# Optimization experiments

Measured on AMD Instinct MI355X. Metric: run time of the kernel, lower is better.

## Reference

```python
import jax, jax.numpy as jnp
import numpy as np

B, K, C = 16384, 128, 32  # batch, feature dim, number of private-label classes
LN2 = 0.6931471805599453


def setup_inputs() -> dict:
    key = jax.random.key(0)
    k1, k2, k3 = jax.random.split(key, 3)
    feature = jax.random.normal(k1, (B, K), dtype=jnp.float32)
    privatelabel = jax.random.randint(k2, (B,), 0, C)
    pan = jax.random.normal(k3, (1,), dtype=jnp.float32)  # unused by the module
    return {"feature": feature, "privatelabel": privatelabel, "pan": pan}


def _privacy_loss(feature, privatelabel):
    b, k = feature.shape
    labels = privatelabel
    onehot = jax.nn.one_hot(labels, C, dtype=feature.dtype)          # [B,C]
    counts = onehot.sum(axis=0)                                      # [C]
    mu = (onehot.T @ feature) / counts[:, None]                      # [C,K] per-class mean
    xc = feature - mu[labels]                                        # [B,K] centered rows
    # per-class scatter: S_c = (1/n_c) * sum_{i in c} xc_i xc_i^T + I
    xw = xc[:, None, :] * onehot[:, :, None]                         # [B,C,K]
    S = jnp.einsum('bci,bj->cij', xw, xc) / counts[:, None, None]
    S = S + jnp.eye(k, dtype=feature.dtype)                          # Sigma_a = I
    # pairwise Gaussian KL (with log base 2, as in the torch code)
    ld2 = jnp.linalg.slogdet(S)[1] / LN2                             # log2 det Sigma_c
    inv = jnp.linalg.inv(S)                                          # [C,K,K]
    diff = mu[:, None, :] - mu[None, :, :]                           # [C,C,K] (i,j)
    quad = jnp.einsum('ijk,jkl,ijl->ij', diff, inv, diff)           # (u1-u2)^T S2^-1 (u1-u2)
    tr = jnp.einsum('jab,iba->ij', inv, S)                           # trace(S2^-1 S1)
    kl = 0.5 * ((ld2[None, :] - ld2[:, None]) - float(k) + quad + tr)
    # dict-insertion key order = order of first occurrence of each label;
    # loops are i in [0, C-2] (rows), j in [1, C-1] (cols) over that order
    first = jnp.full((C,), b, dtype=jnp.int32).at[labels].min(
        jnp.arange(b, dtype=jnp.int32))
    rank = jnp.argsort(jnp.argsort(first))                           # appearance rank per class
    mask = (rank[:, None] <= C - 2) & (rank[None, :] >= 1)
    result = -jnp.sum(mu * mu) + jnp.sum(jnp.where(mask, kl, jnp.zeros_like(kl)))
    return result[None]                                              # shape (1,), like torch


def reference(feature, privatelabel, pan):
    return _privacy_loss(feature, privatelabel)
```

## Files before the change

### kernel.cpp

```cpp
#include <hip/hip_runtime.h>

#define B_ROWS 16384
#define K_DIM  128
#define C_CLS  32

#define O_COUNTS   0
#define O_FIRST    256
#define O_RANK     512
#define O_OFFS     768
#define O_KLACC    1024
#define O_LD2      1152
#define O_COUNTSF  1280
#define O_COLSUM   2048
#define O_MU       18432
#define O_LIST     34816
#define O_S        102400
#define O_PART     (102400 + 2097152)
#define O_INV      O_PART

__global__ __launch_bounds__(1024) void k_bucket(const int* __restrict__ label,
    int* __restrict__ counts, int* __restrict__ rank_g, int* __restrict__ offs,
    float* __restrict__ countsf, int* __restrict__ list) {
  __shared__ int lc[C_CLS], lf[C_CLS], loff[C_CLS], lcur[C_CLS];
  const int t = threadIdx.x;
  if (t < C_CLS) { lc[t] = 0; lf[t] = 0x7fffffff; lcur[t] = 0; }
  __syncthreads();
  #pragma unroll
  for (int q = 0; q < 16; ++q) {
    int i = q * 1024 + t;
    int c = label[i];
    atomicAdd(&lc[c], 1);
    atomicMin(&lf[c], i);
  }
  __syncthreads();
  if (t == 0) {
    int run = 0;
    for (int c = 0; c < C_CLS; ++c) { loff[c] = run; run += lc[c]; }
  }
  __syncthreads();
  if (t < C_CLS) {
    counts[t]  = lc[t];
    countsf[t] = (float)lc[t];
    offs[t]    = loff[t];
    int f = lf[t], r = 0;
    for (int c2 = 0; c2 < C_CLS; ++c2) {
      int f2 = lf[c2];
      r += (f2 < f) || (f2 == f && c2 < t);
    }
    rank_g[t] = r;
  }
  #pragma unroll
  for (int q = 0; q < 16; ++q) {
    int i = q * 1024 + t;
    int c = label[i];
    int pos = atomicAdd(&lcur[c], 1);
    list[loff[c] + pos] = i;
  }
}

__global__ __launch_bounds__(256) void k_scatter(const float* __restrict__ feat,
    const int* __restrict__ counts, const int* __restrict__ offs,
    const int* __restrict__ list, float* __restrict__ part, float* __restrict__ colsum) {
  const int c = blockIdx.x >> 2, s = blockIdx.x & 3;
  const int n = counts[c], off = offs[c];
  const int beg = off + (n * s) / 4, end = off + (n * (s + 1)) / 4;
  __shared__ __align__(16) float ls[32 * 128];
  const int t = threadIdx.x;
  const int tr = t >> 4, tc = t & 15;
  float acc[8][8];
  #pragma unroll
  for (int i = 0; i < 8; ++i)
    #pragma unroll
    for (int j = 0; j < 8; ++j) acc[i][j] = 0.f;
  float cs = 0.f;
  const int col = t & 127, half = t >> 7;
  for (int base = beg; base < end; base += 32) {
    const int nb = min(32, end - base);
    __syncthreads();
    #pragma unroll
    for (int w = 0; w < 4; ++w) {
      int f4 = w * 256 + t;
      int r = f4 >> 5, c4 = f4 & 31;
      float4 v = make_float4(0.f, 0.f, 0.f, 0.f);
      if (r < nb) {
        int row = list[base + r];
        v = ((const float4*)(feat + (long)row * K_DIM))[c4];
      }
      ((float4*)ls)[f4] = v;
    }
    __syncthreads();
    #pragma unroll
    for (int r0 = 0; r0 < 16; ++r0) cs += ls[(half * 16 + r0) * 128 + col];
    for (int r = 0; r < nb; ++r) {
      const float4* lr = (const float4*)(ls + r * 128);
      float4 A0 = lr[tr * 2], A1 = lr[tr * 2 + 1];
      float4 B0 = lr[tc * 2], B1 = lr[tc * 2 + 1];
      float av[8] = {A0.x, A0.y, A0.z, A0.w, A1.x, A1.y, A1.z, A1.w};
      float bv[8] = {B0.x, B0.y, B0.z, B0.w, B1.x, B1.y, B1.z, B1.w};
      #pragma unroll
      for (int i = 0; i < 8; ++i)
        #pragma unroll
        for (int j = 0; j < 8; ++j) acc[i][j] += av[i] * bv[j];
    }
  }
  float* Pc = part + (long)blockIdx.x * 16384;
  #pragma unroll
  for (int i = 0; i < 8; ++i) {
    float4* prow = (float4*)(Pc + (tr * 8 + i) * 128);
    prow[tc * 2]     = make_float4(acc[i][0], acc[i][1], acc[i][2], acc[i][3]);
    prow[tc * 2 + 1] = make_float4(acc[i][4], acc[i][5], acc[i][6], acc[i][7]);
  }
  atomicAdd(&colsum[c * 128 + col], cs);
}

__global__ __launch_bounds__(256) void k_finalize(const float* __restrict__ part,
    float* __restrict__ S, const float* __restrict__ colsum,
    const float* __restrict__ countsf, float* __restrict__ mu) {
  const int c = blockIdx.x, t = threadIdx.x;
  __shared__ __align__(16) float ml[128];
  const float n = countsf[c];
  if (t < 128) {
    float m = colsum[c * 128 + t] / n;
    ml[t] = m;
    mu[c * 128 + t] = m;
  }
  __syncthreads();
  const float4* P0 = (const float4*)(part + (long)(c * 4 + 0) * 16384);
  const float4* P1 = (const float4*)(part + (long)(c * 4 + 1) * 16384);
  const float4* P2 = (const float4*)(part + (long)(c * 4 + 2) * 16384);
  const float4* P3 = (const float4*)(part + (long)(c * 4 + 3) * 16384);
  float4* S4 = (float4*)(S + c * 16384);
  const float rn = 1.0f / n;
  #pragma unroll
  for (int q = 0; q < 16; ++q) {
    int f4 = q * 256 + t;
    int a = f4 >> 5, b = (f4 & 31) * 4;
    float4 v0 = P0[f4], v1 = P1[f4], v2 = P2[f4], v3 = P3[f4];
    float4 v;
    v.x = (v0.x + v1.x) + (v2.x + v3.x);
    v.y = (v0.y + v1.y) + (v2.y + v3.y);
    v.z = (v0.z + v1.z) + (v2.z + v3.z);
    v.w = (v0.w + v1.w) + (v2.w + v3.w);
    float ma = ml[a];
    v.x = v.x * rn - ma * ml[b + 0] + ((a == b + 0) ? 1.f : 0.f);
    v.y = v.y * rn - ma * ml[b + 1] + ((a == b + 1) ? 1.f : 0.f);
    v.z = v.z * rn - ma * ml[b + 2] + ((a == b + 2) ? 1.f : 0.f);
    v.w = v.w * rn - ma * ml[b + 3] + ((a == b + 3) ? 1.f : 0.f);
    S4[f4] = v;
  }
}

__global__ __launch_bounds__(512) void k_sweep(const float* __restrict__ S,
    float* __restrict__ INVg, float* __restrict__ ld2) {
  const int c = blockIdx.x, t = threadIdx.x;
  __shared__ __align__(16) float vbuf[2][132];
  const float4* S4 = (const float4*)(S + c * 16384);
  float4 A[8];
  #pragma unroll
  for (int q = 0; q < 8; ++q) A[q] = S4[q * 512 + t];
  const int h = t >> 5, c4i = t & 31;
  float lda = 0.f;

  for (int P = 0; P < 128; ++P) {
    float* vb = vbuf[P & 1];
    if (h == (P & 15)) {
      const int qexp = P >> 4;
      float4 ex = A[0];
      #pragma unroll
      for (int q = 1; q < 8; ++q) if (q == qexp) ex = A[q];
      if (c4i == (P >> 2)) {
        const int e = P & 3;
        float dv = (e == 0) ? ex.x : (e == 1) ? ex.y : (e == 2) ? ex.z : ex.w;
        vb[128] = dv;
        if (e == 0) ex.x -= 1.f; else if (e == 1) ex.y -= 1.f;
        else if (e == 2) ex.z -= 1.f; else ex.w -= 1.f;
      }
      ((float4*)vb)[c4i] = ex;
    }
    __syncthreads();
    const float d = vb[128];
    const float dinv = 1.0f / d;
    lda += __log2f(d);
    const float4 vc = ((const float4*)vb)[c4i];
    const float4 wc = make_float4(vc.x * dinv, vc.y * dinv, vc.z * dinv, vc.w * dinv);
    #pragma unroll
    for (int q = 0; q < 8; ++q) {
      const float vr = vb[q * 16 + h];
      A[q].x -= vr * wc.x;
      A[q].y -= vr * wc.y;
      A[q].z -= vr * wc.z;
      A[q].w -= vr * wc.w;
    }
  }

  float4* O4 = (float4*)(INVg + c * 16384);
  const int e = h & 3;
  const float4 addv = make_float4(e == 0 ? 2.f : 0.f, e == 1 ? 2.f : 0.f,
                                  e == 2 ? 2.f : 0.f, e == 3 ? 2.f : 0.f);
  #pragma unroll
  for (int q = 0; q < 8; ++q) {
    const int rq = q * 16 + h;
    const float pf = (c4i == (rq >> 2)) ? 1.f : 0.f;
    float4 o;
    o.x = pf * addv.x - A[q].x;
    o.y = pf * addv.y - A[q].y;
    o.z = pf * addv.z - A[q].z;
    o.w = pf * addv.w - A[q].w;
    O4[q * 512 + t] = o;
  }
  if (t == 0) ld2[c] = lda;
}

__global__ __launch_bounds__(256) void k_pairs(const float* __restrict__ S,
    const float* __restrict__ INVg, const float* __restrict__ mu,
    const float* __restrict__ ld2, const int* __restrict__ rank_g,
    float* __restrict__ klacc) {
  const int j = blockIdx.x, i = blockIdx.y;
  if (rank_g[i] > C_CLS - 2 || rank_g[j] < 1) return;
  __shared__ __align__(16) float dl[128];
  __shared__ float wsum[4];
  const int t = threadIdx.x;
  if (t < 128) dl[t] = mu[i * 128 + t] - mu[j * 128 + t];
  __syncthreads();
  const float4* Si4 = (const float4*)(S + i * 16384);
  const float4* Ij4 = (const float4*)(INVg + j * 16384);
  float s = 0.f;
  #pragma unroll
  for (int q = 0; q < 16; ++q) {
    int f4 = q * 256 + t;
    int a = f4 >> 5, b4 = f4 & 31;
    float da = dl[a];
    float4 db = ((const float4*)dl)[b4];
    float4 si = Si4[f4], ij = Ij4[f4];
    s += ij.x * (si.x + da * db.x);
    s += ij.y * (si.y + da * db.y);
    s += ij.z * (si.z + da * db.z);
    s += ij.w * (si.w + da * db.w);
  }
  #pragma unroll
  for (int off = 32; off > 0; off >>= 1) s += __shfl_xor(s, off);
  if ((t & 63) == 0) wsum[t >> 6] = s;
  __syncthreads();
  if (t == 0) {
    float tot = wsum[0] + wsum[1] + wsum[2] + wsum[3];
    float kl = 0.5f * ((ld2[j] - ld2[i]) - 128.0f + tot);
    atomicAdd(klacc, kl);
  }
}

__global__ __launch_bounds__(256) void k_final(const float* __restrict__ mu,
    const float* __restrict__ klacc, float* __restrict__ out) {
  const int t = threadIdx.x;
  __shared__ float wsum[4];
  float s = 0.f;
  #pragma unroll
  for (int q = 0; q < 16; ++q) {
    float m = mu[q * 256 + t];
    s += m * m;
  }
  #pragma unroll
  for (int off = 32; off > 0; off >>= 1) s += __shfl_xor(s, off);
  if ((t & 63) == 0) wsum[t >> 6] = s;
  __syncthreads();
  if (t == 0) out[0] = klacc[0] - (wsum[0] + wsum[1] + wsum[2] + wsum[3]);
}

extern "C" void kernel_launch(void* const* d_in, const int* in_sizes, int n_in,
                              void* d_out, int out_size, void* d_ws, size_t ws_size,
                              hipStream_t stream) {
  const float* feat  = (const float*)d_in[0];
  const int*   label = (const int*)d_in[1];
  float* out = (float*)d_out;
  char*  ws  = (char*)d_ws;

  int*   counts  = (int*)(ws + O_COUNTS);
  int*   rank_g  = (int*)(ws + O_RANK);
  int*   offs    = (int*)(ws + O_OFFS);
  float* klacc   = (float*)(ws + O_KLACC);
  float* ld2     = (float*)(ws + O_LD2);
  float* countsf = (float*)(ws + O_COUNTSF);
  float* colsum  = (float*)(ws + O_COLSUM);
  float* mu      = (float*)(ws + O_MU);
  int*   list    = (int*)(ws + O_LIST);
  float* S       = (float*)(ws + O_S);
  float* part    = (float*)(ws + O_PART);
  float* INVg    = (float*)(ws + O_INV);

  hipMemsetAsync(ws, 0, 18432, stream);

  k_bucket  <<<1,            1024, 0, stream>>>(label, counts, rank_g, offs, countsf, list);
  k_scatter <<<128,           256, 0, stream>>>(feat, counts, offs, list, part, colsum);
  k_finalize<<<C_CLS,         256, 0, stream>>>(part, S, colsum, countsf, mu);
  k_sweep   <<<C_CLS,         512, 0, stream>>>(S, INVg, ld2);
  k_pairs   <<<dim3(C_CLS, C_CLS), 256, 0, stream>>>(S, INVg, mu, ld2, rank_g, klacc);
  k_final   <<<1,             256, 0, stream>>>(mu, klacc, out);
}
```

Before: 180.0 us.

## Fuse label bucketing into scatter blocks and block the Gauss-Jordan sweep by four

New measurement: 201.9 us. 12.1% more time.

```diff
diff --git a/kernel.cpp b/kernel.cpp
--- a/kernel.cpp
+++ b/kernel.cpp
@@ -7,65 +7,52 @@
 #define O_COUNTS   0
 #define O_FIRST    256
 #define O_RANK     512
-#define O_OFFS     768
 #define O_KLACC    1024
 #define O_LD2      1152
-#define O_COUNTSF  1280
 #define O_COLSUM   2048
 #define O_MU       18432
-#define O_LIST     34816
 #define O_S        102400
 #define O_PART     (102400 + 2097152)
 #define O_INV      O_PART
 
-__global__ __launch_bounds__(1024) void k_bucket(const int* __restrict__ label,
-    int* __restrict__ counts, int* __restrict__ rank_g, int* __restrict__ offs,
-    float* __restrict__ countsf, int* __restrict__ list) {
-  __shared__ int lc[C_CLS], lf[C_CLS], loff[C_CLS], lcur[C_CLS];
+__global__ __launch_bounds__(256) void k_init(int* __restrict__ counts,
+    int* __restrict__ first, float* __restrict__ colsum, float* __restrict__ klacc) {
   const int t = threadIdx.x;
-  if (t < C_CLS) { lc[t] = 0; lf[t] = 0x7fffffff; lcur[t] = 0; }
-  __syncthreads();
-  #pragma unroll
-  for (int q = 0; q < 16; ++q) {
-    int i = q * 1024 + t;
-    int c = label[i];
-    atomicAdd(&lc[c], 1);
-    atomicMin(&lf[c], i);
-  }
-  __syncthreads();
-  if (t == 0) {
-    int run = 0;
-    for (int c = 0; c < C_CLS; ++c) { loff[c] = run; run += lc[c]; }
-  }
-  __syncthreads();
-  if (t < C_CLS) {
-    counts[t]  = lc[t];
-    countsf[t] = (float)lc[t];
-    offs[t]    = loff[t];
-    int f = lf[t], r = 0;
-    for (int c2 = 0; c2 < C_CLS; ++c2) {
-      int f2 = lf[c2];
-      r += (f2 < f) || (f2 == f && c2 < t);
-    }
-    rank_g[t] = r;
-  }
-  #pragma unroll
-  for (int q = 0; q < 16; ++q) {
-    int i = q * 1024 + t;
-    int c = label[i];
-    int pos = atomicAdd(&lcur[c], 1);
-    list[loff[c] + pos] = i;
-  }
+  if (t < C_CLS) { counts[t] = 0; first[t] = 0x7fffffff; }
+  if (t == 0) klacc[0] = 0.f;
+  for (int i = t; i < C_CLS * K_DIM; i += 256) colsum[i] = 0.f;
 }
 
 __global__ __launch_bounds__(256) void k_scatter(const float* __restrict__ feat,
-    const int* __restrict__ counts, const int* __restrict__ offs,
-    const int* __restrict__ list, float* __restrict__ part, float* __restrict__ colsum) {
+    const int* __restrict__ label, int* __restrict__ counts, int* __restrict__ first,
+    float* __restrict__ part, float* __restrict__ colsum) {
   const int c = blockIdx.x >> 2, s = blockIdx.x & 3;
-  const int n = counts[c], off = offs[c];
-  const int beg = off + (n * s) / 4, end = off + (n * (s + 1)) / 4;
+  __shared__ int lls[4096];
+  __shared__ int lcnt;
   __shared__ __align__(16) float ls[32 * 128];
   const int t = threadIdx.x;
+  if (t == 0) lcnt = 0;
+  __syncthreads();
+  int myMin = 0x7fffffff;
+  const int lane = t & 63;
+  for (int r0 = 0; r0 < 4096; r0 += 256) {
+    const int i = s * 4096 + r0 + t;
+    const bool match = (label[i] == c);
+    unsigned long long mask = __ballot(match);
+    int prefix = __popcll(mask & ((1ull << lane) - 1ull));
+    int wcnt = __popcll(mask);
+    int base = 0;
+    if (lane == 0 && wcnt) base = atomicAdd(&lcnt, wcnt);
+    base = __shfl(base, 0);
+    if (match) { lls[base + prefix] = i; myMin = min(myMin, i); }
+  }
+  #pragma unroll
+  for (int off = 32; off > 0; off >>= 1) myMin = min(myMin, __shfl_xor(myMin, off));
+  if (lane == 0 && myMin != 0x7fffffff) atomicMin(&first[c], myMin);
+  __syncthreads();
+  const int n = lcnt;
+  if (t == 0) atomicAdd(&counts[c], n);
+
   const int tr = t >> 4, tc = t & 15;
   float acc[8][8];
   #pragma unroll
@@ -74,8 +61,8 @@
     for (int j = 0; j < 8; ++j) acc[i][j] = 0.f;
   float cs = 0.f;
   const int col = t & 127, half = t >> 7;
-  for (int base = beg; base < end; base += 32) {
-    const int nb = min(32, end - base);
+  for (int base2 = 0; base2 < n; base2 += 32) {
+    const int nb = min(32, n - base2);
     __syncthreads();
     #pragma unroll
     for (int w = 0; w < 4; ++w) {
@@ -83,7 +70,7 @@
       int r = f4 >> 5, c4 = f4 & 31;
       float4 v = make_float4(0.f, 0.f, 0.f, 0.f);
       if (r < nb) {
-        int row = list[base + r];
+        int row = lls[base2 + r];
         v = ((const float4*)(feat + (long)row * K_DIM))[c4];
       }
       ((float4*)ls)[f4] = v;
@@ -115,14 +102,24 @@
 
 __global__ __launch_bounds__(256) void k_finalize(const float* __restrict__ part,
     float* __restrict__ S, const float* __restrict__ colsum,
-    const float* __restrict__ countsf, float* __restrict__ mu) {
+    const int* __restrict__ counts, const int* __restrict__ first,
+    float* __restrict__ mu, int* __restrict__ rank_g) {
   const int c = blockIdx.x, t = threadIdx.x;
   __shared__ __align__(16) float ml[128];
-  const float n = countsf[c];
+  const float n = (float)counts[c];
   if (t < 128) {
     float m = colsum[c * 128 + t] / n;
     ml[t] = m;
     mu[c * 128 + t] = m;
+  }
+  if (t == 0) {
+    const int f = first[c];
+    int r = 0;
+    for (int c2 = 0; c2 < C_CLS; ++c2) {
+      const int f2 = first[c2];
+      r += (f2 < f) || (f2 == f && c2 < c);
+    }
+    rank_g[c] = r;
   }
   __syncthreads();
   const float4* P0 = (const float4*)(part + (long)(c * 4 + 0) * 16384);
@@ -153,7 +150,7 @@
 __global__ __launch_bounds__(512) void k_sweep(const float* __restrict__ S,
     float* __restrict__ INVg, float* __restrict__ ld2) {
   const int c = blockIdx.x, t = threadIdx.x;
-  __shared__ __align__(16) float vbuf[2][132];
+  __shared__ __align__(16) float pan[2][4][128];
   const float4* S4 = (const float4*)(S + c * 16384);
   float4 A[8];
   #pragma unroll
@@ -161,53 +158,95 @@
   const int h = t >> 5, c4i = t & 31;
   float lda = 0.f;
 
-  for (int P = 0; P < 128; ++P) {
-    float* vb = vbuf[P & 1];
-    if (h == (P & 15)) {
-      const int qexp = P >> 4;
+  for (int P = 0; P < 32; ++P) {
+    float (*Rp)[128] = pan[P & 1];
+    const int qexp = P >> 2;
+    const int hbase = (4 * P) & 15;
+    const int u0 = h - hbase;
+    if ((unsigned)u0 < 4u) {
       float4 ex = A[0];
       #pragma unroll
       for (int q = 1; q < 8; ++q) if (q == qexp) ex = A[q];
-      if (c4i == (P >> 2)) {
-        const int e = P & 3;
-        float dv = (e == 0) ? ex.x : (e == 1) ? ex.y : (e == 2) ? ex.z : ex.w;
-        vb[128] = dv;
-        if (e == 0) ex.x -= 1.f; else if (e == 1) ex.y -= 1.f;
-        else if (e == 2) ex.z -= 1.f; else ex.w -= 1.f;
-      }
-      ((float4*)vb)[c4i] = ex;
+      ((float4*)Rp[u0])[c4i] = ex;
     }
     __syncthreads();
-    const float d = vb[128];
-    const float dinv = 1.0f / d;
-    lda += __log2f(d);
-    const float4 vc = ((const float4*)vb)[c4i];
-    const float4 wc = make_float4(vc.x * dinv, vc.y * dinv, vc.z * dinv, vc.w * dinv);
+    float m[4][4];
+    #pragma unroll
+    for (int u = 0; u < 4; ++u) {
+      float4 dr = ((const float4*)Rp[u])[P];
+      m[u][0] = dr.x; m[u][1] = dr.y; m[u][2] = dr.z; m[u][3] = dr.w;
+    }
+    #pragma unroll
+    for (int p = 0; p < 4; ++p) {
+      const float d = m[p][p];
+      const float dinv = 1.0f / d;
+      lda += __log2f(d);
+      #pragma unroll
+      for (int r = 0; r < 4; ++r) {
+        if (r != p) {
+          #pragma unroll
+          for (int cc = 0; cc < 4; ++cc)
+            if (cc != p) m[r][cc] -= m[r][p] * m[p][cc] * dinv;
+        }
+      }
+      #pragma unroll
+      for (int cc = 0; cc < 4; ++cc) if (cc != p) m[p][cc] *= dinv;
+      #pragma unroll
+      for (int r = 0; r < 4; ++r) if (r != p) m[r][p] *= dinv;
+      m[p][p] = -dinv;
+    }
+    float4 Rv[4], E[4];
+    #pragma unroll
+    for (int v = 0; v < 4; ++v) Rv[v] = ((const float4*)Rp[v])[c4i];
+    #pragma unroll
+    for (int u = 0; u < 4; ++u) {
+      float4 e = make_float4(0.f, 0.f, 0.f, 0.f);
+      #pragma unroll
+      for (int v = 0; v < 4; ++v) {
+        const float dv = -m[u][v];
+        e.x += dv * Rv[v].x; e.y += dv * Rv[v].y;
+        e.z += dv * Rv[v].z; e.w += dv * Rv[v].w;
+      }
+      E[u] = e;
+    }
+    const bool colp = (c4i == P);
     #pragma unroll
     for (int q = 0; q < 8; ++q) {
-      const float vr = vb[q * 16 + h];
-      A[q].x -= vr * wc.x;
-      A[q].y -= vr * wc.y;
-      A[q].z -= vr * wc.z;
-      A[q].w -= vr * wc.w;
+      const int rq = q * 16 + h;
+      const float cr0 = Rp[0][rq], cr1 = Rp[1][rq];
+      const float cr2 = Rp[2][rq], cr3 = Rp[3][rq];
+      float4 a = A[q];
+      a.x -= cr0 * E[0].x + cr1 * E[1].x + cr2 * E[2].x + cr3 * E[3].x;
+      a.y -= cr0 * E[0].y + cr1 * E[1].y + cr2 * E[2].y + cr3 * E[3].y;
+      a.z -= cr0 * E[0].z + cr1 * E[1].z + cr2 * E[2].z + cr3 * E[3].z;
+      a.w -= cr0 * E[0].w + cr1 * E[1].w + cr2 * E[2].w + cr3 * E[3].w;
+      if (colp) {
+        a.x = -(cr0 * m[0][0] + cr1 * m[1][0] + cr2 * m[2][0] + cr3 * m[3][0]);
+        a.y = -(cr0 * m[0][1] + cr1 * m[1][1] + cr2 * m[2][1] + cr3 * m[3][1]);
+        a.z = -(cr0 * m[0][2] + cr1 * m[1][2] + cr2 * m[2][2] + cr3 * m[3][2]);
+        a.w = -(cr0 * m[0][3] + cr1 * m[1][3] + cr2 * m[2][3] + cr3 * m[3][3]);
+      }
+      A[q] = a;
+    }
+    if ((unsigned)u0 < 4u) {
+      float4 ev = E[0];
+      #pragma unroll
+      for (int u = 1; u < 4; ++u) if (u == u0) ev = E[u];
+      if (colp) {
+        ev = make_float4(m[0][0], m[0][1], m[0][2], m[0][3]);
+        #pragma unroll
+        for (int u = 1; u < 4; ++u)
+          if (u == u0) ev = make_float4(m[u][0], m[u][1], m[u][2], m[u][3]);
+      }
+      #pragma unroll
+      for (int q = 0; q < 8; ++q) if (q == qexp) A[q] = ev;
     }
   }
 
   float4* O4 = (float4*)(INVg + c * 16384);
-  const int e = h & 3;
-  const float4 addv = make_float4(e == 0 ? 2.f : 0.f, e == 1 ? 2.f : 0.f,
-                                  e == 2 ? 2.f : 0.f, e == 3 ? 2.f : 0.f);
-  #pragma unroll
-  for (int q = 0; q < 8; ++q) {
-    const int rq = q * 16 + h;
-    const float pf = (c4i == (rq >> 2)) ? 1.f : 0.f;
-    float4 o;
-    o.x = pf * addv.x - A[q].x;
-    o.y = pf * addv.y - A[q].y;
-    o.z = pf * addv.z - A[q].z;
-    o.w = pf * addv.w - A[q].w;
-    O4[q * 512 + t] = o;
-  }
+  #pragma unroll
+  for (int q = 0; q < 8; ++q)
+    O4[q * 512 + t] = make_float4(-A[q].x, -A[q].y, -A[q].z, -A[q].w);
   if (t == 0) ld2[c] = lda;
 }
 
@@ -274,23 +313,19 @@
   char*  ws  = (char*)d_ws;
 
   int*   counts  = (int*)(ws + O_COUNTS);
+  int*   first   = (int*)(ws + O_FIRST);
   int*   rank_g  = (int*)(ws + O_RANK);
-  int*   offs    = (int*)(ws + O_OFFS);
   float* klacc   = (float*)(ws + O_KLACC);
   float* ld2     = (float*)(ws + O_LD2);
-  float* countsf = (float*)(ws + O_COUNTSF);
   float* colsum  = (float*)(ws + O_COLSUM);
   float* mu      = (float*)(ws + O_MU);
-  int*   list    = (int*)(ws + O_LIST);
   float* S       = (float*)(ws + O_S);
   float* part    = (float*)(ws + O_PART);
   float* INVg    = (float*)(ws + O_INV);
 
-  hipMemsetAsync(ws, 0, 18432, stream);
-
-  k_bucket  <<<1,            1024, 0, stream>>>(label, counts, rank_g, offs, countsf, list);
-  k_scatter <<<128,           256, 0, stream>>>(feat, counts, offs, list, part, colsum);
-  k_finalize<<<C_CLS,         256, 0, stream>>>(part, S, colsum, countsf, mu);
+  k_init    <<<1,             256, 0, stream>>>(counts, first, colsum, klacc);
+  k_scatter <<<128,           256, 0, stream>>>(feat, label, counts, first, part, colsum);
+  k_finalize<<<C_CLS,         256, 0, stream>>>(part, S, colsum, counts, first, mu, rank_g);
   k_sweep   <<<C_CLS,         512, 0, stream>>>(S, INVg, ld2);
   k_pairs   <<<dim3(C_CLS, C_CLS), 256, 0, stream>>>(S, INVg, mu, ld2, rank_g, klacc);
   k_final   <<<1,             256, 0, stream>>>(mu, klacc, out);
```

## Fuse bucketing into scatter, merge finalize with sweep, drop final kernel

Applied to the files above, without the earlier changes.

Measured after the change: 159.6 us. 1.13x faster.

```diff
diff --git a/kernel.cpp b/kernel.cpp
--- a/kernel.cpp
+++ b/kernel.cpp
@@ -7,65 +7,53 @@
 #define O_COUNTS   0
 #define O_FIRST    256
 #define O_RANK     512
-#define O_OFFS     768
-#define O_KLACC    1024
 #define O_LD2      1152
-#define O_COUNTSF  1280
 #define O_COLSUM   2048
 #define O_MU       18432
-#define O_LIST     34816
 #define O_S        102400
 #define O_PART     (102400 + 2097152)
 #define O_INV      O_PART
 
-__global__ __launch_bounds__(1024) void k_bucket(const int* __restrict__ label,
-    int* __restrict__ counts, int* __restrict__ rank_g, int* __restrict__ offs,
-    float* __restrict__ countsf, int* __restrict__ list) {
-  __shared__ int lc[C_CLS], lf[C_CLS], loff[C_CLS], lcur[C_CLS];
+__global__ __launch_bounds__(256) void k_init(int* __restrict__ counts,
+    int* __restrict__ first, float* __restrict__ colsum, float* __restrict__ out) {
   const int t = threadIdx.x;
-  if (t < C_CLS) { lc[t] = 0; lf[t] = 0x7fffffff; lcur[t] = 0; }
-  __syncthreads();
-  #pragma unroll
-  for (int q = 0; q < 16; ++q) {
-    int i = q * 1024 + t;
-    int c = label[i];
-    atomicAdd(&lc[c], 1);
-    atomicMin(&lf[c], i);
-  }
-  __syncthreads();
-  if (t == 0) {
-    int run = 0;
-    for (int c = 0; c < C_CLS; ++c) { loff[c] = run; run += lc[c]; }
-  }
-  __syncthreads();
-  if (t < C_CLS) {
-    counts[t]  = lc[t];
-    countsf[t] = (float)lc[t];
-    offs[t]    = loff[t];
-    int f = lf[t], r = 0;
-    for (int c2 = 0; c2 < C_CLS; ++c2) {
-      int f2 = lf[c2];
-      r += (f2 < f) || (f2 == f && c2 < t);
-    }
-    rank_g[t] = r;
-  }
-  #pragma unroll
-  for (int q = 0; q < 16; ++q) {
-    int i = q * 1024 + t;
-    int c = label[i];
-    int pos = atomicAdd(&lcur[c], 1);
-    list[loff[c] + pos] = i;
-  }
-}
-
+  if (t < C_CLS) { counts[t] = 0; first[t] = 0x7fffffff; }
+  if (t == 0) out[0] = 0.f;
+  for (int i = t; i < C_CLS * K_DIM; i += 256) colsum[i] = 0.f;
+}
+
+template<int NSPLIT>
 __global__ __launch_bounds__(256) void k_scatter(const float* __restrict__ feat,
-    const int* __restrict__ counts, const int* __restrict__ offs,
-    const int* __restrict__ list, float* __restrict__ part, float* __restrict__ colsum) {
-  const int c = blockIdx.x >> 2, s = blockIdx.x & 3;
-  const int n = counts[c], off = offs[c];
-  const int beg = off + (n * s) / 4, end = off + (n * (s + 1)) / 4;
+    const int* __restrict__ label, int* __restrict__ counts, int* __restrict__ first,
+    float* __restrict__ part, float* __restrict__ colsum) {
+  constexpr int CH = B_ROWS / NSPLIT;
+  const int c = blockIdx.x / NSPLIT, s = blockIdx.x % NSPLIT;
+  __shared__ int lls[CH];
+  __shared__ int lcnt;
   __shared__ __align__(16) float ls[32 * 128];
   const int t = threadIdx.x;
+  if (t == 0) lcnt = 0;
+  __syncthreads();
+  int myMin = 0x7fffffff;
+  const int lane = t & 63;
+  for (int r0 = 0; r0 < CH; r0 += 256) {
+    const int i = s * CH + r0 + t;
+    const bool match = (label[i] == c);
+    unsigned long long mask = __ballot(match);
+    int prefix = __popcll(mask & ((1ull << lane) - 1ull));
+    int wcnt = __popcll(mask);
+    int base = 0;
+    if (lane == 0 && wcnt) base = atomicAdd(&lcnt, wcnt);
+    base = __shfl(base, 0);
+    if (match) { lls[base + prefix] = i; myMin = min(myMin, i); }
+  }
+  #pragma unroll
+  for (int off = 32; off > 0; off >>= 1) myMin = min(myMin, __shfl_xor(myMin, off));
+  if (lane == 0 && myMin != 0x7fffffff) atomicMin(&first[c], myMin);
+  __syncthreads();
+  const int n = lcnt;
+  if (t == 0) atomicAdd(&counts[c], n);
+
   const int tr = t >> 4, tc = t & 15;
   float acc[8][8];
   #pragma unroll
@@ -74,8 +62,8 @@
     for (int j = 0; j < 8; ++j) acc[i][j] = 0.f;
   float cs = 0.f;
   const int col = t & 127, half = t >> 7;
-  for (int base = beg; base < end; base += 32) {
-    const int nb = min(32, end - base);
+  for (int base2 = 0; base2 < n; base2 += 32) {
+    const int nb = min(32, n - base2);
     __syncthreads();
     #pragma unroll
     for (int w = 0; w < 4; ++w) {
@@ -83,7 +71,7 @@
       int r = f4 >> 5, c4 = f4 & 31;
       float4 v = make_float4(0.f, 0.f, 0.f, 0.f);
       if (r < nb) {
-        int row = list[base + r];
+        int row = lls[base2 + r];
         v = ((const float4*)(feat + (long)row * K_DIM))[c4];
       }
       ((float4*)ls)[f4] = v;
@@ -113,61 +101,62 @@
   atomicAdd(&colsum[c * 128 + col], cs);
 }
 
-__global__ __launch_bounds__(256) void k_finalize(const float* __restrict__ part,
-    float* __restrict__ S, const float* __restrict__ colsum,
-    const float* __restrict__ countsf, float* __restrict__ mu) {
+template<int NSPLIT>
+__global__ __launch_bounds__(1024) void k_sweepf(const float* __restrict__ part,
+    const float* __restrict__ colsum, const int* __restrict__ counts,
+    const int* __restrict__ first, float* __restrict__ S, float* __restrict__ INVg,
+    float* __restrict__ mu, int* __restrict__ rank_g, float* __restrict__ ld2) {
   const int c = blockIdx.x, t = threadIdx.x;
   __shared__ __align__(16) float ml[128];
-  const float n = countsf[c];
+  __shared__ __align__(16) float vbuf[2][132];
+  const float n = (float)counts[c];
+  const float rn = 1.0f / n;
   if (t < 128) {
-    float m = colsum[c * 128 + t] / n;
+    float m = colsum[c * 128 + t] * rn;
     ml[t] = m;
     mu[c * 128 + t] = m;
   }
-  __syncthreads();
-  const float4* P0 = (const float4*)(part + (long)(c * 4 + 0) * 16384);
-  const float4* P1 = (const float4*)(part + (long)(c * 4 + 1) * 16384);
-  const float4* P2 = (const float4*)(part + (long)(c * 4 + 2) * 16384);
-  const float4* P3 = (const float4*)(part + (long)(c * 4 + 3) * 16384);
+  if (t == 0) {
+    const int f = first[c];
+    int r = 0;
+    for (int c2 = 0; c2 < C_CLS; ++c2) {
+      const int f2 = first[c2];
+      r += (f2 < f) || (f2 == f && c2 < c);
+    }
+    rank_g[c] = r;
+  }
+  __syncthreads();
+  const int h = t >> 5, c4i = t & 31;
+  float4 A[4];
   float4* S4 = (float4*)(S + c * 16384);
-  const float rn = 1.0f / n;
-  #pragma unroll
-  for (int q = 0; q < 16; ++q) {
-    int f4 = q * 256 + t;
-    int a = f4 >> 5, b = (f4 & 31) * 4;
-    float4 v0 = P0[f4], v1 = P1[f4], v2 = P2[f4], v3 = P3[f4];
-    float4 v;
-    v.x = (v0.x + v1.x) + (v2.x + v3.x);
-    v.y = (v0.y + v1.y) + (v2.y + v3.y);
-    v.z = (v0.z + v1.z) + (v2.z + v3.z);
-    v.w = (v0.w + v1.w) + (v2.w + v3.w);
-    float ma = ml[a];
-    v.x = v.x * rn - ma * ml[b + 0] + ((a == b + 0) ? 1.f : 0.f);
-    v.y = v.y * rn - ma * ml[b + 1] + ((a == b + 1) ? 1.f : 0.f);
-    v.z = v.z * rn - ma * ml[b + 2] + ((a == b + 2) ? 1.f : 0.f);
-    v.w = v.w * rn - ma * ml[b + 3] + ((a == b + 3) ? 1.f : 0.f);
+  #pragma unroll
+  for (int q = 0; q < 4; ++q) {
+    const int f4 = q * 1024 + t;
+    float4 v = make_float4(0.f, 0.f, 0.f, 0.f);
+    #pragma unroll
+    for (int k = 0; k < NSPLIT; ++k) {
+      const float4 p = ((const float4*)(part + (long)(c * NSPLIT + k) * 16384))[f4];
+      v.x += p.x; v.y += p.y; v.z += p.z; v.w += p.w;
+    }
+    const int row = q * 32 + h;
+    const float mr = ml[row];
+    const float4 mc = ((const float4*)ml)[c4i];
+    const int b = 4 * c4i;
+    v.x = v.x * rn - mr * mc.x + ((row == b + 0) ? 1.f : 0.f);
+    v.y = v.y * rn - mr * mc.y + ((row == b + 1) ? 1.f : 0.f);
+    v.z = v.z * rn - mr * mc.z + ((row == b + 2) ? 1.f : 0.f);
+    v.w = v.w * rn - mr * mc.w + ((row == b + 3) ? 1.f : 0.f);
+    A[q] = v;
     S4[f4] = v;
   }
-}
-
-__global__ __launch_bounds__(512) void k_sweep(const float* __restrict__ S,
-    float* __restrict__ INVg, float* __restrict__ ld2) {
-  const int c = blockIdx.x, t = threadIdx.x;
-  __shared__ __align__(16) float vbuf[2][132];
-  const float4* S4 = (const float4*)(S + c * 16384);
-  float4 A[8];
-  #pragma unroll
-  for (int q = 0; q < 8; ++q) A[q] = S4[q * 512 + t];
-  const int h = t >> 5, c4i = t & 31;
   float lda = 0.f;
-
   for (int P = 0; P < 128; ++P) {
     float* vb = vbuf[P & 1];
-    if (h == (P & 15)) {
-      const int qexp = P >> 4;
+    if (h == (P & 31)) {
+      const int qexp = P >> 5;
       float4 ex = A[0];
       #pragma unroll
-      for (int q = 1; q < 8; ++q) if (q == qexp) ex = A[q];
+      for (int q = 1; q < 4; ++q) if (q == qexp) ex = A[q];
       if (c4i == (P >> 2)) {
         const int e = P & 3;
         float dv = (e == 0) ? ex.x : (e == 1) ? ex.y : (e == 2) ? ex.z : ex.w;
@@ -184,29 +173,26 @@
     const float4 vc = ((const float4*)vb)[c4i];
     const float4 wc = make_float4(vc.x * dinv, vc.y * dinv, vc.z * dinv, vc.w * dinv);
     #pragma unroll
-    for (int q = 0; q < 8; ++q) {
-      const float vr = vb[q * 16 + h];
+    for (int q = 0; q < 4; ++q) {
+      const float vr = vb[q * 32 + h];
       A[q].x -= vr * wc.x;
       A[q].y -= vr * wc.y;
       A[q].z -= vr * wc.z;
       A[q].w -= vr * wc.w;
     }
   }
-
   float4* O4 = (float4*)(INVg + c * 16384);
   const int e = h & 3;
-  const float4 addv = make_float4(e == 0 ? 2.f : 0.f, e == 1 ? 2.f : 0.f,
-                                  e == 2 ? 2.f : 0.f, e == 3 ? 2.f : 0.f);
-  #pragma unroll
-  for (int q = 0; q < 8; ++q) {
-    const int rq = q * 16 + h;
-    const float pf = (c4i == (rq >> 2)) ? 1.f : 0.f;
+  #pragma unroll
+  for (int q = 0; q < 4; ++q) {
+    const int rq = q * 32 + h;
+    const float pf = (c4i == (rq >> 2)) ? 2.f : 0.f;
     float4 o;
-    o.x = pf * addv.x - A[q].x;
-    o.y = pf * addv.y - A[q].y;
-    o.z = pf * addv.z - A[q].z;
-    o.w = pf * addv.w - A[q].w;
-    O4[q * 512 + t] = o;
+    o.x = ((e == 0) ? pf : 0.f) - A[q].x;
+    o.y = ((e == 1) ? pf : 0.f) - A[q].y;
+    o.z = ((e == 2) ? pf : 0.f) - A[q].z;
+    o.w = ((e == 3) ? pf : 0.f) - A[q].w;
+    O4[q * 1024 + t] = o;
   }
   if (t == 0) ld2[c] = lda;
 }
@@ -214,12 +200,23 @@
 __global__ __launch_bounds__(256) void k_pairs(const float* __restrict__ S,
     const float* __restrict__ INVg, const float* __restrict__ mu,
     const float* __restrict__ ld2, const int* __restrict__ rank_g,
-    float* __restrict__ klacc) {
+    float* __restrict__ out) {
   const int j = blockIdx.x, i = blockIdx.y;
-  if (rank_g[i] > C_CLS - 2 || rank_g[j] < 1) return;
+  const int t = threadIdx.x;
   __shared__ __align__(16) float dl[128];
   __shared__ float wsum[4];
-  const int t = threadIdx.x;
+  if (i == 0 && j == 0) {
+    float s2 = 0.f;
+    #pragma unroll
+    for (int q = 0; q < 16; ++q) { float m = mu[q * 256 + t]; s2 += m * m; }
+    #pragma unroll
+    for (int off = 32; off > 0; off >>= 1) s2 += __shfl_xor(s2, off);
+    if ((t & 63) == 0) wsum[t >> 6] = s2;
+    __syncthreads();
+    if (t == 0) atomicAdd(out, -(wsum[0] + wsum[1] + wsum[2] + wsum[3]));
+    __syncthreads();
+  }
+  if (rank_g[i] > C_CLS - 2 || rank_g[j] < 1) return;
   if (t < 128) dl[t] = mu[i * 128 + t] - mu[j * 128 + t];
   __syncthreads();
   const float4* Si4 = (const float4*)(S + i * 16384);
@@ -244,25 +241,8 @@
   if (t == 0) {
     float tot = wsum[0] + wsum[1] + wsum[2] + wsum[3];
     float kl = 0.5f * ((ld2[j] - ld2[i]) - 128.0f + tot);
-    atomicAdd(klacc, kl);
-  }
-}
-
-__global__ __launch_bounds__(256) void k_final(const float* __restrict__ mu,
-    const float* __restrict__ klacc, float* __restrict__ out) {
-  const int t = threadIdx.x;
-  __shared__ float wsum[4];
-  float s = 0.f;
-  #pragma unroll
-  for (int q = 0; q < 16; ++q) {
-    float m = mu[q * 256 + t];
-    s += m * m;
-  }
-  #pragma unroll
-  for (int off = 32; off > 0; off >>= 1) s += __shfl_xor(s, off);
-  if ((t & 63) == 0) wsum[t >> 6] = s;
-  __syncthreads();
-  if (t == 0) out[0] = klacc[0] - (wsum[0] + wsum[1] + wsum[2] + wsum[3]);
+    atomicAdd(out, kl);
+  }
 }
 
 extern "C" void kernel_launch(void* const* d_in, const int* in_sizes, int n_in,
@@ -274,24 +254,24 @@
   char*  ws  = (char*)d_ws;
 
   int*   counts  = (int*)(ws + O_COUNTS);
+  int*   first   = (int*)(ws + O_FIRST);
   int*   rank_g  = (int*)(ws + O_RANK);
-  int*   offs    = (int*)(ws + O_OFFS);
-  float* klacc   = (float*)(ws + O_KLACC);
   float* ld2     = (float*)(ws + O_LD2);
-  float* countsf = (float*)(ws + O_COUNTSF);
   float* colsum  = (float*)(ws + O_COLSUM);
   float* mu      = (float*)(ws + O_MU);
-  int*   list    = (int*)(ws + O_LIST);
   float* S       = (float*)(ws + O_S);
   float* part    = (float*)(ws + O_PART);
   float* INVg    = (float*)(ws + O_INV);
 
-  hipMemsetAsync(ws, 0, 18432, stream);
-
-  k_bucket  <<<1,            1024, 0, stream>>>(label, counts, rank_g, offs, countsf, list);
-  k_scatter <<<128,           256, 0, stream>>>(feat, counts, offs, list, part, colsum);
-  k_finalize<<<C_CLS,         256, 0, stream>>>(part, S, colsum, countsf, mu);
-  k_sweep   <<<C_CLS,         512, 0, stream>>>(S, INVg, ld2);
-  k_pairs   <<<dim3(C_CLS, C_CLS), 256, 0, stream>>>(S, INVg, mu, ld2, rank_g, klacc);
-  k_final   <<<1,             256, 0, stream>>>(mu, klacc, out);
-}
+  const size_t need8 = (size_t)O_PART + (size_t)C_CLS * 8 * 65536;
+
+  k_init<<<1, 256, 0, stream>>>(counts, first, colsum, out);
+  if (ws_size >= need8) {
+    k_scatter<8><<<C_CLS * 8, 256,  0, stream>>>(feat, label, counts, first, part, colsum);
+    k_sweepf<8> <<<C_CLS,     1024, 0, stream>>>(part, colsum, counts, first, S, INVg, mu, rank_g, ld2);
+  } else {
+    k_scatter<4><<<C_CLS * 4, 256,  0, stream>>>(feat, label, counts, first, part, colsum);
+    k_sweepf<4> <<<C_CLS,     1024, 0, stream>>>(part, colsum, counts, first, S, INVg, mu, rank_g, ld2);
+  }
+  k_pairs<<<dim3(C_CLS, C_CLS), 256, 0, stream>>>(S, INVg, mu, ld2, rank_g, out);
+}
```
